# Kernel optimization log

Measured on AMD Instinct MI355X. Metric: run time of the kernel, lower is better.

Reference implementation:

```python
import jax, jax.numpy as jnp
import numpy as np

B, T, I, H, O = 256, 512, 64, 512, 1


def setup_inputs() -> dict:
    key = jax.random.key(0)
    ks = jax.random.split(key, 8)
    s_ih = 1.0 / np.sqrt(H)
    inp = {
        "x": jax.random.normal(ks[0], (B, T, I), dtype=jnp.float32),
        "W_ih": jax.random.uniform(ks[1], (4 * H, I), minval=-s_ih, maxval=s_ih, dtype=jnp.float32),
        "W_hh": jax.random.uniform(ks[2], (4 * H, H), minval=-s_ih, maxval=s_ih, dtype=jnp.float32),
        "b_ih": jax.random.uniform(ks[3], (4 * H,), minval=-s_ih, maxval=s_ih, dtype=jnp.float32),
        "b_hh": jax.random.uniform(ks[4], (4 * H,), minval=-s_ih, maxval=s_ih, dtype=jnp.float32),
        "W_fc": jax.random.uniform(ks[5], (O, H), minval=-s_ih, maxval=s_ih, dtype=jnp.float32),
        "b_fc": jax.random.uniform(ks[6], (O,), minval=-s_ih, maxval=s_ih, dtype=jnp.float32),
    }
    return inp


def _lstm_last_h(x, W_ih, W_hh, b_ih, b_hh):
    # x: [B, T, I]. Precompute input projection for all timesteps (one big GEMM).
    x_gates = jnp.einsum("bti,gi->btg", x, W_ih) + b_ih + b_hh  # [B, T, 4H]
    x_gates = jnp.swapaxes(x_gates, 0, 1)  # [T, B, 4H] for scan
    hdim = W_hh.shape[1]
    h0 = jnp.zeros((x.shape[0], hdim), dtype=x.dtype)
    c0 = jnp.zeros((x.shape[0], hdim), dtype=x.dtype)

    def step(carry, xg):
        h, c = carry
        gates = xg + h @ W_hh.T  # [B, 4H]
        i, f, g, o = jnp.split(gates, 4, axis=-1)  # PyTorch gate order: i, f, g, o
        i = jax.nn.sigmoid(i)
        f = jax.nn.sigmoid(f)
        g = jnp.tanh(g)
        o = jax.nn.sigmoid(o)
        c = f * c + i * g
        h = o * jnp.tanh(c)
        return (h, c), None

    (h_last, _), _ = jax.lax.scan(step, (h0, c0), x_gates)
    return h_last  # [B, H] == out[:, -1, :] for a single-layer LSTM


def reference(x, W_ih, W_hh, b_ih, b_hh, W_fc, b_fc):
    h_last = _lstm_last_h(x, W_ih, W_hh, b_ih, b_hh)
    return h_last @ W_fc.T + b_fc  # [B, O]
```

## Files before the change

kernel.cpp:

```cpp
#include <hip/hip_runtime.h>

typedef _Float16 h8 __attribute__((ext_vector_type(8)));
typedef float v4f __attribute__((ext_vector_type(4)));

#define B_  256
#define T_  512
#define I_  64
#define H_  512

#define OFF_W16   0
#define OFF_WIH   (OFF_W16 + 2048*512*2)
#define OFF_BIAS  (OFF_WIH + 2048*64*2)
#define OFF_X16   (OFF_BIAS + 2048*4)
#define OFF_H0    (OFF_X16 + 512*256*64*2)
#define OFF_H1    (OFF_H0 + 256*512*2)
#define OFF_CTR   (OFF_H1 + 256*512*2)

__device__ __forceinline__ float sigf(float x) {
    float e = __builtin_amdgcn_exp2f(-1.442695041f * x);
    return __builtin_amdgcn_rcpf(1.f + e);
}
__device__ __forceinline__ float tanhf_(float x) {
    float e = __builtin_amdgcn_exp2f(2.885390082f * x);
    return 1.f - 2.f * __builtin_amdgcn_rcpf(e + 1.f);
}

union Pack4 { _Float16 f[4]; unsigned long long u; };

__global__ void prep_w(const float* __restrict__ Wih, const float* __restrict__ Whh,
                       const float* __restrict__ bih, const float* __restrict__ bhh,
                       _Float16* __restrict__ W16, _Float16* __restrict__ Wih16,
                       float* __restrict__ bias, _Float16* __restrict__ h0,
                       unsigned* __restrict__ ctr) {
    int idx = blockIdx.x * 256 + threadIdx.x;
    W16[idx] = (_Float16)Whh[idx];
    if (idx < 2048 * 64)  Wih16[idx] = (_Float16)Wih[idx];
    if (idx < 2048)       bias[idx] = bih[idx] + bhh[idx];
    if (idx < 32768)
        __hip_atomic_store((unsigned long long*)h0 + idx, 0ull,
                           __ATOMIC_RELAXED, __HIP_MEMORY_SCOPE_AGENT);
    if (idx < 128)
        __hip_atomic_store(ctr + idx, 0u, __ATOMIC_RELAXED, __HIP_MEMORY_SCOPE_AGENT);
}

__global__ void prep_x(const float* __restrict__ x, _Float16* __restrict__ x16) {
    int idx = blockIdx.x * 256 + threadIdx.x;
    int t = idx >> 14;
    int rem = idx & 16383;
    int b = rem >> 6;
    int i = rem & 63;
    x16[idx] = (_Float16)x[((size_t)b * T_ + t) * I_ + i];
}

__launch_bounds__(256, 1)
__global__ void lstm_k(const _Float16* __restrict__ W16, const _Float16* __restrict__ Wih16,
                       const float* __restrict__ bias, const _Float16* __restrict__ x16,
                       _Float16* __restrict__ h0, _Float16* __restrict__ h1,
                       unsigned* __restrict__ ctr) {
    __shared__ _Float16 Als[18][33][40];
    __shared__ float    S[32][132];

    const int tid  = threadIdx.x;
    const int lane = tid & 63;
    const int wave = tid >> 6;
    const int bg = blockIdx.x & 7;
    const int cg = blockIdx.x >> 3;
    const int B0 = bg * 32;
    const int J0 = cg * 32;
    const int r  = lane & 15;
    const int q  = lane >> 4;

    h8 bfrag[2][18];
    float biasv[2];
#pragma unroll
    for (int t = 0; t < 2; ++t) {
        const int wrow = wave * H_ + J0 + t * 16 + r;
#pragma unroll
        for (int kk = 0; kk < 16; ++kk)
            bfrag[t][kk] = *(const h8*)(W16 + (size_t)wrow * H_ + kk * 32 + q * 8);
#pragma unroll
        for (int kk = 16; kk < 18; ++kk)
            bfrag[t][kk] = *(const h8*)(Wih16 + (size_t)wrow * I_ + (kk - 16) * 32 + q * 8);
        biasv[t] = bias[wrow];
    }

    const int er = tid >> 3;
    const int ec = (tid & 7) * 4;
    float c[4] = {0.f, 0.f, 0.f, 0.f};

    unsigned* myctr = ctr + bg * 16;

    const int xrow = tid >> 3, xs8 = tid & 7;
    h8 xv = *(const h8*)(x16 + ((size_t)B0 + xrow) * I_ + xs8 * 8);

    for (int s = 0; s < T_; ++s) {
        const _Float16* hp = (s & 1) ? h1 : h0;
        _Float16*       hn = (s & 1) ? h0 : h1;

        {
            const unsigned long long* hp64 =
                (const unsigned long long*)(hp + (size_t)B0 * H_);
            unsigned long long hv[16];
#pragma unroll
            for (int it = 0; it < 16; ++it)
                hv[it] = __hip_atomic_load(hp64 + tid + 256 * it,
                                           __ATOMIC_RELAXED, __HIP_MEMORY_SCOPE_AGENT);
            *(h8*)&Als[16 + (xs8 >> 2)][xrow][(xs8 & 3) * 8] = xv;
#pragma unroll
            for (int it = 0; it < 16; ++it) {
                int n = tid + 256 * it;
                *(unsigned long long*)&Als[(n & 127) >> 3][n >> 7][(n & 7) * 4] = hv[it];
            }
        }
        __syncthreads();

        v4f a00 = {0,0,0,0}, a01 = {0,0,0,0}, a10 = {0,0,0,0}, a11 = {0,0,0,0};
#pragma unroll
        for (int kk = 0; kk < 18; ++kk) {
            h8 am0 = *(const h8*)&Als[kk][r][q * 8];
            h8 am1 = *(const h8*)&Als[kk][16 + r][q * 8];
            a00 = __builtin_amdgcn_mfma_f32_16x16x32_f16(am0, bfrag[0][kk], a00, 0, 0, 0);
            a01 = __builtin_amdgcn_mfma_f32_16x16x32_f16(am1, bfrag[0][kk], a01, 0, 0, 0);
            a10 = __builtin_amdgcn_mfma_f32_16x16x32_f16(am0, bfrag[1][kk], a10, 0, 0, 0);
            a11 = __builtin_amdgcn_mfma_f32_16x16x32_f16(am1, bfrag[1][kk], a11, 0, 0, 0);
        }
#pragma unroll
        for (int reg = 0; reg < 4; ++reg) {
            S[q * 4 + reg][wave * 32 + r]           = a00[reg] + biasv[0];
            S[16 + q * 4 + reg][wave * 32 + r]      = a01[reg] + biasv[0];
            S[q * 4 + reg][wave * 32 + 16 + r]      = a10[reg] + biasv[1];
            S[16 + q * 4 + reg][wave * 32 + 16 + r] = a11[reg] + biasv[1];
        }
        __syncthreads();

        {
            Pack4 pk;
#pragma unroll
            for (int j = 0; j < 3 + 1; ++j) {
                float iv = sigf  (S[er][ec + j]);
                float fv = sigf  (S[er][32 + ec + j]);
                float gv = tanhf_(S[er][64 + ec + j]);
                float ov = sigf  (S[er][96 + ec + j]);
                c[j] = fv * c[j] + iv * gv;
                pk.f[j] = (_Float16)(ov * tanhf_(c[j]));
            }
            __hip_atomic_store(
                (unsigned long long*)(hn + ((size_t)B0 + er) * H_ + J0 + ec),
                pk.u, __ATOMIC_RELAXED, __HIP_MEMORY_SCOPE_AGENT);
        }
        __syncthreads();

        if (tid == 0)
            __hip_atomic_fetch_add(myctr, 1u, __ATOMIC_RELAXED, __HIP_MEMORY_SCOPE_AGENT);
        if (s + 1 < T_)
            xv = *(const h8*)(x16 + (((size_t)(s + 1)) * B_ + B0 + xrow) * I_ + xs8 * 8);
        if (tid == 0) {
            const unsigned target = 16u * (unsigned)(s + 1);
            int guard = 0;
            while (__hip_atomic_load(myctr, __ATOMIC_RELAXED, __HIP_MEMORY_SCOPE_AGENT) < target) {
                __builtin_amdgcn_s_sleep(1);
                if (++guard > (1 << 17)) break;
            }
        }
        __syncthreads();
    }
}

__global__ void fc_k(const _Float16* __restrict__ hlast, const float* __restrict__ Wfc,
                     const float* __restrict__ bfc, float* __restrict__ out) {
    int b = blockIdx.x;
    int lane = threadIdx.x;
    const unsigned long long* hp64 = (const unsigned long long*)(hlast + (size_t)b * H_);
    Pack4 p0, p1;
    p0.u = __hip_atomic_load(hp64 + lane * 2,     __ATOMIC_RELAXED, __HIP_MEMORY_SCOPE_AGENT);
    p1.u = __hip_atomic_load(hp64 + lane * 2 + 1, __ATOMIC_RELAXED, __HIP_MEMORY_SCOPE_AGENT);
    float sum = 0.f;
#pragma unroll
    for (int j = 0; j < 4; ++j) sum += (float)p0.f[j] * Wfc[lane * 8 + j];
#pragma unroll
    for (int j = 0; j < 4; ++j) sum += (float)p1.f[j] * Wfc[lane * 8 + 4 + j];
    for (int off = 32; off; off >>= 1) sum += __shfl_down(sum, off);
    if (lane == 0) out[b] = sum + bfc[0];
}

extern "C" void kernel_launch(void* const* d_in, const int* in_sizes, int n_in,
                              void* d_out, int out_size, void* d_ws, size_t ws_size,
                              hipStream_t stream) {
    (void)in_sizes; (void)n_in; (void)out_size; (void)ws_size;
    const float* x   = (const float*)d_in[0];
    const float* Wih = (const float*)d_in[1];
    const float* Whh = (const float*)d_in[2];
    const float* bih = (const float*)d_in[3];
    const float* bhh = (const float*)d_in[4];
    const float* Wfc = (const float*)d_in[5];
    const float* bfc = (const float*)d_in[6];
    float* out = (float*)d_out;

    char* ws = (char*)d_ws;
    _Float16* W16   = (_Float16*)(ws + OFF_W16);
    _Float16* Wih16 = (_Float16*)(ws + OFF_WIH);
    float*    biasf = (float*)(ws + OFF_BIAS);
    _Float16* x16   = (_Float16*)(ws + OFF_X16);
    _Float16* h0b   = (_Float16*)(ws + OFF_H0);
    _Float16* h1b   = (_Float16*)(ws + OFF_H1);
    unsigned* ctrb  = (unsigned*)(ws + OFF_CTR);

    hipLaunchKernelGGL(prep_w, dim3((2048 * 512) / 256), dim3(256), 0, stream,
                       Wih, Whh, bih, bhh, W16, Wih16, biasf, h0b, ctrb);
    hipLaunchKernelGGL(prep_x, dim3((512 * 256 * 64) / 256), dim3(256), 0, stream, x, x16);
    hipLaunchKernelGGL(lstm_k, dim3(128), dim3(256), 0, stream,
                       W16, Wih16, biasf, x16, h0b, h1b, ctrb);
    hipLaunchKernelGGL(fc_k, dim3(256), dim3(64), 0, stream, h0b, Wfc, bfc, out);
}
```

Before: 1.503 ms.

## Replace counter barrier with step-tagged hidden-state words and per-word polling

Drops the per-step atomic counter barrier and its extra __syncthreads. Each h value pair is now packed with a 32-bit timestep tag into a 64-bit word, so consumers spin on the data itself until every tag matches the current step. The hidden-state layout becomes column-pair-major per batch group, and waves are remapped so each wave handles 16 rows across two gates, with a vectorized transposed gate buffer. This removes a global round-trip and a block-wide sync per step. In exchange it doubles the bytes loaded per step and adds polling traffic on many words.

```diff
diff --git a/kernel.cpp b/kernel.cpp
--- a/kernel.cpp
+++ b/kernel.cpp
@@ -2,6 +2,7 @@
 
 typedef _Float16 h8 __attribute__((ext_vector_type(8)));
 typedef float v4f __attribute__((ext_vector_type(4)));
+typedef unsigned long long ull;
 
 #define B_  256
 #define T_  512
@@ -12,9 +13,7 @@
 #define OFF_WIH   (OFF_W16 + 2048*512*2)
 #define OFF_BIAS  (OFF_WIH + 2048*64*2)
 #define OFF_X16   (OFF_BIAS + 2048*4)
-#define OFF_H0    (OFF_X16 + 512*256*64*2)
-#define OFF_H1    (OFF_H0 + 256*512*2)
-#define OFF_CTR   (OFF_H1 + 256*512*2)
+#define OFF_HPK   (OFF_X16 + 512*256*64*2)
 
 __device__ __forceinline__ float sigf(float x) {
     float e = __builtin_amdgcn_exp2f(-1.442695041f * x);
@@ -25,22 +24,18 @@
     return 1.f - 2.f * __builtin_amdgcn_rcpf(e + 1.f);
 }
 
-union Pack4 { _Float16 f[4]; unsigned long long u; };
+union P2 { _Float16 f[2]; unsigned u; };
 
 __global__ void prep_w(const float* __restrict__ Wih, const float* __restrict__ Whh,
                        const float* __restrict__ bih, const float* __restrict__ bhh,
                        _Float16* __restrict__ W16, _Float16* __restrict__ Wih16,
-                       float* __restrict__ bias, _Float16* __restrict__ h0,
-                       unsigned* __restrict__ ctr) {
+                       float* __restrict__ bias, ull* __restrict__ hpk) {
     int idx = blockIdx.x * 256 + threadIdx.x;
     W16[idx] = (_Float16)Whh[idx];
     if (idx < 2048 * 64)  Wih16[idx] = (_Float16)Wih[idx];
     if (idx < 2048)       bias[idx] = bih[idx] + bhh[idx];
-    if (idx < 32768)
-        __hip_atomic_store((unsigned long long*)h0 + idx, 0ull,
-                           __ATOMIC_RELAXED, __HIP_MEMORY_SCOPE_AGENT);
-    if (idx < 128)
-        __hip_atomic_store(ctr + idx, 0u, __ATOMIC_RELAXED, __HIP_MEMORY_SCOPE_AGENT);
+    if (idx < 65536)
+        __hip_atomic_store(hpk + idx, 0ull, __ATOMIC_RELAXED, __HIP_MEMORY_SCOPE_AGENT);
 }
 
 __global__ void prep_x(const float* __restrict__ x, _Float16* __restrict__ x16) {
@@ -55,10 +50,9 @@
 __launch_bounds__(256, 1)
 __global__ void lstm_k(const _Float16* __restrict__ W16, const _Float16* __restrict__ Wih16,
                        const float* __restrict__ bias, const _Float16* __restrict__ x16,
-                       _Float16* __restrict__ h0, _Float16* __restrict__ h1,
-                       unsigned* __restrict__ ctr) {
-    __shared__ _Float16 Als[18][33][40];
-    __shared__ float    S[32][132];
+                       ull* __restrict__ hpk) {
+    __shared__ _Float16 Als[18][32][36];
+    __shared__ float    Sg[128][36];
 
     const int tid  = threadIdx.x;
     const int lane = tid & 63;
@@ -67,118 +61,141 @@
     const int cg = blockIdx.x >> 3;
     const int B0 = bg * 32;
     const int J0 = cg * 32;
+    const int m  = wave & 1;
+    const int gp = (wave >> 1) * 2;
     const int r  = lane & 15;
     const int q  = lane >> 4;
-
-    h8 bfrag[2][18];
-    float biasv[2];
-#pragma unroll
-    for (int t = 0; t < 2; ++t) {
-        const int wrow = wave * H_ + J0 + t * 16 + r;
+    const int m16 = m * 16;
+    const int q8  = q * 8;
+
+    h8 bf[4][18];
+    float biasv[4];
+#pragma unroll
+    for (int gi = 0; gi < 2; ++gi)
+#pragma unroll
+    for (int ct = 0; ct < 2; ++ct) {
+        const int t = gi * 2 + ct;
+        const int wrow = (gp + gi) * H_ + J0 + ct * 16 + r;
 #pragma unroll
         for (int kk = 0; kk < 16; ++kk)
-            bfrag[t][kk] = *(const h8*)(W16 + (size_t)wrow * H_ + kk * 32 + q * 8);
+            bf[t][kk] = *(const h8*)(W16 + (size_t)wrow * H_ + kk * 32 + q8);
 #pragma unroll
         for (int kk = 16; kk < 18; ++kk)
-            bfrag[t][kk] = *(const h8*)(Wih16 + (size_t)wrow * I_ + (kk - 16) * 32 + q * 8);
+            bf[t][kk] = *(const h8*)(Wih16 + (size_t)wrow * I_ + (kk - 16) * 32 + q8);
         biasv[t] = bias[wrow];
     }
 
-    const int er = tid >> 3;
-    const int ec = (tid & 7) * 4;
+    const int crow = tid & 31;
+    const int cch  = tid >> 5;
+    const int er = tid & 31;
+    const int ec = (tid >> 5) * 4;
     float c[4] = {0.f, 0.f, 0.f, 0.f};
-
-    unsigned* myctr = ctr + bg * 16;
-
     const int xrow = tid >> 3, xs8 = tid & 7;
-    h8 xv = *(const h8*)(x16 + ((size_t)B0 + xrow) * I_ + xs8 * 8);
+
+    ull* hbase = hpk + bg * 8192;
 
     for (int s = 0; s < T_; ++s) {
-        const _Float16* hp = (s & 1) ? h1 : h0;
-        _Float16*       hn = (s & 1) ? h0 : h1;
-
         {
-            const unsigned long long* hp64 =
-                (const unsigned long long*)(hp + (size_t)B0 * H_);
-            unsigned long long hv[16];
-#pragma unroll
-            for (int it = 0; it < 16; ++it)
-                hv[it] = __hip_atomic_load(hp64 + tid + 256 * it,
-                                           __ATOMIC_RELAXED, __HIP_MEMORY_SCOPE_AGENT);
-            *(h8*)&Als[16 + (xs8 >> 2)][xrow][(xs8 & 3) * 8] = xv;
-#pragma unroll
-            for (int it = 0; it < 16; ++it) {
-                int n = tid + 256 * it;
-                *(unsigned long long*)&Als[(n & 127) >> 3][n >> 7][(n & 7) * 4] = hv[it];
-            }
+            const ull* src = hbase + (size_t)(s & 1) * 65536;
+            const int pb0 = cch * 16;
+            const int pb1 = (cch + 8) * 16;
+            ull v[32];
+#pragma unroll
+            for (int j = 0; j < 16; ++j)
+                v[j] = __hip_atomic_load(src + (pb0 + j) * 32 + crow,
+                                         __ATOMIC_RELAXED, __HIP_MEMORY_SCOPE_AGENT);
+#pragma unroll
+            for (int j = 0; j < 16; ++j)
+                v[16 + j] = __hip_atomic_load(src + (pb1 + j) * 32 + crow,
+                                              __ATOMIC_RELAXED, __HIP_MEMORY_SCOPE_AGENT);
+            h8 xv = *(const h8*)(x16 + ((size_t)s * B_ + B0 + xrow) * I_ + xs8 * 8);
+
+            const unsigned tg = (unsigned)s;
+            for (int guard = 0; guard < (1 << 18); ++guard) {
+                bool all = true;
+#pragma unroll
+                for (int j = 0; j < 32; ++j) {
+                    if ((unsigned)(v[j] >> 32) != tg) {
+                        all = false;
+                        const int p = (j < 16) ? (pb0 + j) : (pb1 + j - 16);
+                        v[j] = __hip_atomic_load(src + p * 32 + crow,
+                                                 __ATOMIC_RELAXED, __HIP_MEMORY_SCOPE_AGENT);
+                    }
+                }
+                if (all) break;
+            }
+#pragma unroll
+            for (int j = 0; j < 8; ++j) {
+                ull w0 = (ull)(unsigned)v[2*j] | ((ull)(unsigned)v[2*j+1] << 32);
+                *(ull*)&Als[cch][crow][j * 4] = w0;
+            }
+#pragma unroll
+            for (int j = 0; j < 8; ++j) {
+                ull w1 = (ull)(unsigned)v[16+2*j] | ((ull)(unsigned)v[16+2*j+1] << 32);
+                *(ull*)&Als[cch + 8][crow][j * 4] = w1;
+            }
+            union { h8 v; ull u[2]; } xa; xa.v = xv;
+            *(ull*)&Als[16 + (xs8 >> 2)][xrow][(xs8 & 3) * 8]     = xa.u[0];
+            *(ull*)&Als[16 + (xs8 >> 2)][xrow][(xs8 & 3) * 8 + 4] = xa.u[1];
         }
         __syncthreads();
 
-        v4f a00 = {0,0,0,0}, a01 = {0,0,0,0}, a10 = {0,0,0,0}, a11 = {0,0,0,0};
+        v4f acc[4] = {{0,0,0,0},{0,0,0,0},{0,0,0,0},{0,0,0,0}};
 #pragma unroll
         for (int kk = 0; kk < 18; ++kk) {
-            h8 am0 = *(const h8*)&Als[kk][r][q * 8];
-            h8 am1 = *(const h8*)&Als[kk][16 + r][q * 8];
-            a00 = __builtin_amdgcn_mfma_f32_16x16x32_f16(am0, bfrag[0][kk], a00, 0, 0, 0);
-            a01 = __builtin_amdgcn_mfma_f32_16x16x32_f16(am1, bfrag[0][kk], a01, 0, 0, 0);
-            a10 = __builtin_amdgcn_mfma_f32_16x16x32_f16(am0, bfrag[1][kk], a10, 0, 0, 0);
-            a11 = __builtin_amdgcn_mfma_f32_16x16x32_f16(am1, bfrag[1][kk], a11, 0, 0, 0);
-        }
-#pragma unroll
-        for (int reg = 0; reg < 4; ++reg) {
-            S[q * 4 + reg][wave * 32 + r]           = a00[reg] + biasv[0];
-            S[16 + q * 4 + reg][wave * 32 + r]      = a01[reg] + biasv[0];
-            S[q * 4 + reg][wave * 32 + 16 + r]      = a10[reg] + biasv[1];
-            S[16 + q * 4 + reg][wave * 32 + 16 + r] = a11[reg] + biasv[1];
+            union { h8 v; ull u[2]; } a;
+            a.u[0] = *(const ull*)&Als[kk][m16 + r][q8];
+            a.u[1] = *(const ull*)&Als[kk][m16 + r][q8 + 4];
+            acc[0] = __builtin_amdgcn_mfma_f32_16x16x32_f16(a.v, bf[0][kk], acc[0], 0, 0, 0);
+            acc[1] = __builtin_amdgcn_mfma_f32_16x16x32_f16(a.v, bf[1][kk], acc[1], 0, 0, 0);
+            acc[2] = __builtin_amdgcn_mfma_f32_16x16x32_f16(a.v, bf[2][kk], acc[2], 0, 0, 0);
+            acc[3] = __builtin_amdgcn_mfma_f32_16x16x32_f16(a.v, bf[3][kk], acc[3], 0, 0, 0);
+        }
+#pragma unroll
+        for (int gi = 0; gi < 2; ++gi)
+#pragma unroll
+        for (int ct = 0; ct < 2; ++ct) {
+            const int t = gi * 2 + ct;
+            v4f vv = acc[t] + biasv[t];
+            *(v4f*)&Sg[(gp + gi) * 32 + ct * 16 + r][m16 + q * 4] = vv;
         }
         __syncthreads();
 
         {
-            Pack4 pk;
-#pragma unroll
-            for (int j = 0; j < 3 + 1; ++j) {
-                float iv = sigf  (S[er][ec + j]);
-                float fv = sigf  (S[er][32 + ec + j]);
-                float gv = tanhf_(S[er][64 + ec + j]);
-                float ov = sigf  (S[er][96 + ec + j]);
+            ull* dst = hbase + (size_t)((s + 1) & 1) * 65536;
+            const int pc = cg * 16 + (ec >> 1);
+            const ull tagbits = ((ull)(unsigned)(s + 1)) << 32;
+            P2 p0, p1;
+#pragma unroll
+            for (int j = 0; j < 4; ++j) {
+                float iv = sigf  (Sg[      ec + j][er]);
+                float fv = sigf  (Sg[ 32 + ec + j][er]);
+                float gv = tanhf_(Sg[ 64 + ec + j][er]);
+                float ov = sigf  (Sg[ 96 + ec + j][er]);
                 c[j] = fv * c[j] + iv * gv;
-                pk.f[j] = (_Float16)(ov * tanhf_(c[j]));
-            }
-            __hip_atomic_store(
-                (unsigned long long*)(hn + ((size_t)B0 + er) * H_ + J0 + ec),
-                pk.u, __ATOMIC_RELAXED, __HIP_MEMORY_SCOPE_AGENT);
-        }
-        __syncthreads();
-
-        if (tid == 0)
-            __hip_atomic_fetch_add(myctr, 1u, __ATOMIC_RELAXED, __HIP_MEMORY_SCOPE_AGENT);
-        if (s + 1 < T_)
-            xv = *(const h8*)(x16 + (((size_t)(s + 1)) * B_ + B0 + xrow) * I_ + xs8 * 8);
-        if (tid == 0) {
-            const unsigned target = 16u * (unsigned)(s + 1);
-            int guard = 0;
-            while (__hip_atomic_load(myctr, __ATOMIC_RELAXED, __HIP_MEMORY_SCOPE_AGENT) < target) {
-                __builtin_amdgcn_s_sleep(1);
-                if (++guard > (1 << 17)) break;
-            }
-        }
-        __syncthreads();
+                float hv = ov * tanhf_(c[j]);
+                if (j < 2) p0.f[j] = (_Float16)hv; else p1.f[j - 2] = (_Float16)hv;
+            }
+            __hip_atomic_store(dst + (pc + 0) * 32 + er, (ull)p0.u | tagbits,
+                               __ATOMIC_RELAXED, __HIP_MEMORY_SCOPE_AGENT);
+            __hip_atomic_store(dst + (pc + 1) * 32 + er, (ull)p1.u | tagbits,
+                               __ATOMIC_RELAXED, __HIP_MEMORY_SCOPE_AGENT);
+        }
     }
 }
 
-__global__ void fc_k(const _Float16* __restrict__ hlast, const float* __restrict__ Wfc,
+__global__ void fc_k(const ull* __restrict__ hpk, const float* __restrict__ Wfc,
                      const float* __restrict__ bfc, float* __restrict__ out) {
     int b = blockIdx.x;
     int lane = threadIdx.x;
-    const unsigned long long* hp64 = (const unsigned long long*)(hlast + (size_t)b * H_);
-    Pack4 p0, p1;
-    p0.u = __hip_atomic_load(hp64 + lane * 2,     __ATOMIC_RELAXED, __HIP_MEMORY_SCOPE_AGENT);
-    p1.u = __hip_atomic_load(hp64 + lane * 2 + 1, __ATOMIC_RELAXED, __HIP_MEMORY_SCOPE_AGENT);
+    const ull* src = hpk + (size_t)(b >> 5) * 8192 + (b & 31);
     float sum = 0.f;
 #pragma unroll
-    for (int j = 0; j < 4; ++j) sum += (float)p0.f[j] * Wfc[lane * 8 + j];
-#pragma unroll
-    for (int j = 0; j < 4; ++j) sum += (float)p1.f[j] * Wfc[lane * 8 + 4 + j];
+    for (int u = 0; u < 4; ++u) {
+        int p = lane * 4 + u;
+        P2 pk; pk.u = (unsigned)src[p * 32];
+        sum += (float)pk.f[0] * Wfc[2 * p] + (float)pk.f[1] * Wfc[2 * p + 1];
+    }
     for (int off = 32; off; off >>= 1) sum += __shfl_down(sum, off);
     if (lane == 0) out[b] = sum + bfc[0];
 }
@@ -201,14 +218,12 @@
     _Float16* Wih16 = (_Float16*)(ws + OFF_WIH);
     float*    biasf = (float*)(ws + OFF_BIAS);
     _Float16* x16   = (_Float16*)(ws + OFF_X16);
-    _Float16* h0b   = (_Float16*)(ws + OFF_H0);
-    _Float16* h1b   = (_Float16*)(ws + OFF_H1);
-    unsigned* ctrb  = (unsigned*)(ws + OFF_CTR);
+    ull*      hpk   = (ull*)(ws + OFF_HPK);
 
     hipLaunchKernelGGL(prep_w, dim3((2048 * 512) / 256), dim3(256), 0, stream,
-                       Wih, Whh, bih, bhh, W16, Wih16, biasf, h0b, ctrb);
+                       Wih, Whh, bih, bhh, W16, Wih16, biasf, hpk);
     hipLaunchKernelGGL(prep_x, dim3((512 * 256 * 64) / 256), dim3(256), 0, stream, x, x16);
     hipLaunchKernelGGL(lstm_k, dim3(128), dim3(256), 0, stream,
-                       W16, Wih16, biasf, x16, h0b, h1b, ctrb);
-    hipLaunchKernelGGL(fc_k, dim3(256), dim3(64), 0, stream, h0b, Wfc, bfc, out);
-}
+                       W16, Wih16, biasf, x16, hpk);
+    hipLaunchKernelGGL(fc_k, dim3(256), dim3(64), 0, stream, hpk, Wfc, bfc, out);
+}
```

Measured after the change: 2.613 ms. 1.74x slower.
